# Kernel tuning notes

Hardware: AMD Instinct MI355X
Metric: run time of the kernel (lower is better)

The kernel has to match this reference:

```python
import jax, jax.numpy as jnp
import numpy as np
import math

ALPHA, BETA = 0.0, 0.1  # MarketRelation defaults


def setup_inputs() -> dict:
    key = jax.random.key(0)
    ks = jax.random.split(key, 15)
    n, T, d, K, C = 1024, 8, 64, 8, 64
    h = d  # hidden = (2*infeat)//2 = infeat
    s = 0.1
    u = jax.random.uniform(ks[13], (n, n, K), jnp.float32, 1e-6, 1.0 - 1e-6)
    return {
        "x":   jax.random.normal(ks[0], (n, T, d), jnp.float32),
        "Ind": jax.random.uniform(ks[1], (n, n), jnp.float32),
        "Loc": jax.random.uniform(ks[2], (n, n), jnp.float32),
        "a":   jax.random.normal(ks[3], (T, 1), jnp.float32),
        "W1m": jax.random.normal(ks[4], (2 * d, h), jnp.float32) * s,
        "b1m": jax.random.normal(ks[5], (h,), jnp.float32) * s,
        "W2m": jax.random.normal(ks[6], (h, 1), jnp.float32) * s,
        "b2m": jax.random.normal(ks[7], (1,), jnp.float32) * s,
        "W1s": jax.random.normal(ks[8], (2 * d, h), jnp.float32) * s,
        "b1s": jax.random.normal(ks[9], (h,), jnp.float32) * s,
        "W2s": jax.random.normal(ks[10], (h, K), jnp.float32) * s,
        "b2s": jax.random.normal(ks[11], (K,), jnp.float32) * s,
        "E":   jax.random.normal(ks[12], (K, n, C), jnp.float32) * s,
        "g":   -jnp.log(-jnp.log(u)),  # Gumbel(0,1) noise for gumbel_softmax
    }


def reference(x, Ind, Loc, a, W1m, b1m, W2m, b2m, W1s, b1s, W2s, b2s, E, g):
    n, T, d = x.shape
    # --- MarketRelation ---
    # fc1(concat(x_j, x_k)) == x_j @ W1m[:d] + x_k @ W1m[d:] + b1m (same math,
    # avoids materializing the N x N x 2d concat tensor)
    W1a, W1b = W1m[:d], W1m[d:]
    a_soft = jax.nn.softmax(a, axis=0)  # [T,1]
    A_mkt = jnp.zeros((n, n), x.dtype)
    for i in range(T):
        xi = x[:, i, :]                      # [n,d]
        hA = xi @ W1a                        # [n,h]
        hB = xi @ W1b                        # [n,h]
        hmat = jax.nn.relu(hA[:, None, :] + hB[None, :, :] + b1m)  # [n,n,h]
        adj = jax.nn.relu(hmat @ W2m + b2m)[..., 0]                # [n,n]
        factor = 1.0 + ALPHA * math.exp(-BETA * (T - i - 1))
        A_mkt = A_mkt + adj * (a_soft[i, 0] * factor)
    # --- NobsRelation (on last timestep) ---
    xl = x[:, -1, :]
    Ws1a, Ws1b = W1s[:d], W1s[d:]
    hs = jax.nn.relu((xl @ Ws1a)[:, None, :] + (xl @ Ws1b)[None, :, :] + b1s)
    logits = jax.nn.relu(hs @ W2s + b2s)          # [n,n,K]
    y = jax.nn.softmax(logits + g, axis=-1)       # gumbel_softmax, tau=1, soft
    D = jnp.einsum('knc,kmc->nmk', E, E)          # stack of E_k E_k^T, [n,n,K]
    A_nobs = jnp.sum(D * y, axis=-1)              # [n,n]
    return jnp.stack([Ind, Loc, A_mkt, A_nobs])   # [4,n,n]
```

## Files before the change

kernel.cpp:

```cpp
#include <hip/hip_runtime.h>

typedef unsigned short USH;
typedef float v2f __attribute__((ext_vector_type(2)));

__device__ __forceinline__ float bf2f(USH u) {
    return __uint_as_float(((unsigned int)u) << 16);
}
__device__ __forceinline__ USH f2bf(float f) {
    unsigned int i = __float_as_uint(f);
    i += 0x7FFFu + ((i >> 16) & 1u);
    return (USH)(i >> 16);
}
__device__ __forceinline__ v2f relu2(v2f s) {
    return __builtin_elementwise_max(s, (v2f)(0.0f));
}

__device__ __forceinline__ float ldf(const void* p, long idx, int bf) {
    return bf ? bf2f(((const USH*)p)[idx]) : ((const float*)p)[idx];
}
__device__ __forceinline__ void ld4(const void* p, long idx, int bf, float o[4]) {
    if (bf) {
        ushort4 u = *(const ushort4*)((const USH*)p + idx);
        o[0] = bf2f(u.x); o[1] = bf2f(u.y); o[2] = bf2f(u.z); o[3] = bf2f(u.w);
    } else {
        float4 v = *(const float4*)((const float*)p + idx);
        o[0] = v.x; o[1] = v.y; o[2] = v.z; o[3] = v.w;
    }
}

__device__ __forceinline__ int detect_bf(const void* ind) {
    const uint4* p = (const uint4*)ind;
    unsigned o = 0;
    #pragma unroll
    for (int i = 0; i < 8; ++i) { uint4 v = p[i]; o |= v.x | v.y | v.z | v.w; }
    return (o & 0x8000u) == 0;
}


__global__ __launch_bounds__(256) void k_pre_d(
    const void* __restrict__ x,
    const void* __restrict__ W1m,
    const void* __restrict__ b1m,
    const void* __restrict__ W1s,
    const void* __restrict__ b1s,
    const void* __restrict__ E,
    const void* __restrict__ IndDet,
    float* __restrict__ hAf,
    float* __restrict__ hBf,
    USH* __restrict__ D)
{
    __shared__ float smem[8192];
    float* sA = smem;
    float* sB = smem + 4096;
    const int bf = detect_bf(IndDet);
    const int tid = threadIdx.x;
    const int bid = blockIdx.x;
    const int tx = tid & 15, ty = tid >> 4;

    if (bid < 2048) {
        const int mb = (bid & 15) * 64, nb = ((bid >> 4) & 15) * 64, k = bid >> 8;
        const long ek = (long)k * 65536;
        {
            const int r_l = tid >> 2, cq = tid & 3;
            const long bn = ek + (long)(nb + r_l) * 64 + cq * 16;
            const long bm = ek + (long)(mb + r_l) * 64 + cq * 16;
            #pragma unroll
            for (int j = 0; j < 4; ++j) {
                const int c0 = cq * 16 + j * 4;
                float o[4];
                ld4(E, bn + j * 4, bf, o);
                #pragma unroll
                for (int e = 0; e < 4; ++e) sA[(c0 + e) * 64 + r_l] = o[e];
                ld4(E, bm + j * 4, bf, o);
                #pragma unroll
                for (int e = 0; e < 4; ++e) sB[(c0 + e) * 64 + r_l] = o[e];
            }
        }
        __syncthreads();
        const int m0 = tx * 4, n0 = ty * 4;
        v2f acc2[4][2] = {};
        #pragma unroll 8
        for (int c = 0; c < 64; ++c) {
            const float4 an = *(const float4*)&sA[c * 64 + n0];
            const float4 am = *(const float4*)&sB[c * 64 + m0];
            const float aa[4] = {an.x, an.y, an.z, an.w};
            v2f m01; m01.x = am.x; m01.y = am.y;
            v2f m23; m23.x = am.z; m23.y = am.w;
            #pragma unroll
            for (int ni = 0; ni < 4; ++ni) {
                const v2f av = (v2f)(aa[ni]);
                acc2[ni][0] = __builtin_elementwise_fma(av, m01, acc2[ni][0]);
                acc2[ni][1] = __builtin_elementwise_fma(av, m23, acc2[ni][1]);
            }
        }
        #pragma unroll
        for (int ni = 0; ni < 4; ++ni) {
            ushort4 o;
            o.x = f2bf(acc2[ni][0].x); o.y = f2bf(acc2[ni][0].y);
            o.z = f2bf(acc2[ni][1].x); o.w = f2bf(acc2[ni][1].y);
            *(ushort4*)&D[(long)k * 1048576 + (long)(nb + n0 + ni) * 1024 + mb + m0] = o;
        }
    } else {
        const int bid2 = bid - 2048;
        const int nbase = (bid2 & 15) * 64;
        const int by = bid2 >> 4;
        int t, rb;
        const void* Wsrc;
        const void* bias;
        float* dst;
        if (by < 8)        { t = by;     rb = 0;  Wsrc = W1m; bias = nullptr; dst = hAf + by * 65536; }
        else if (by < 16)  { t = by - 8; rb = 64; Wsrc = W1m; bias = b1m;     dst = hBf + (by - 8) * 65536; }
        else if (by == 16) { t = 7;      rb = 0;  Wsrc = W1s; bias = nullptr; dst = hAf + 8 * 65536; }
        else               { t = 7;      rb = 64; Wsrc = W1s; bias = b1s;     dst = hBf + 8 * 65536; }

        {
            const int n_l = tid >> 2, dq = tid & 3;
            const long base = (long)(nbase + n_l) * 512 + t * 64 + dq * 16;
            #pragma unroll
            for (int j = 0; j < 4; ++j) {
                float o[4]; ld4(x, base + j * 4, bf, o);
                const int d0 = dq * 16 + j * 4;
                #pragma unroll
                for (int e = 0; e < 4; ++e) sA[(d0 + e) * 64 + n_l] = o[e];
            }
        }
        {
            const int d_l = tid >> 2, cq = tid & 3;
            const long base = (long)(rb + d_l) * 64 + cq * 16;
            #pragma unroll
            for (int j = 0; j < 4; ++j) {
                float o[4]; ld4(Wsrc, base + j * 4, bf, o);
                const int c0 = cq * 16 + j * 4;
                #pragma unroll
                for (int e = 0; e < 4; ++e) sB[d_l * 64 + c0 + e] = o[e];
            }
        }
        __syncthreads();

        const int c0 = tx * 4, nq = ty * 4;
        float acc[4][4] = {};
        #pragma unroll 16
        for (int d = 0; d < 64; ++d) {
            const float4 xa = *(const float4*)&sA[d * 64 + nq];
            const float4 wv = *(const float4*)&sB[d * 64 + c0];
            const float aa[4] = {xa.x, xa.y, xa.z, xa.w};
            const float ww[4] = {wv.x, wv.y, wv.z, wv.w};
            #pragma unroll
            for (int ci = 0; ci < 4; ++ci)
                #pragma unroll
                for (int ni = 0; ni < 4; ++ni)
                    acc[ci][ni] += ww[ci] * aa[ni];
        }
        float b[4] = {0.f, 0.f, 0.f, 0.f};
        if (bias) {
            #pragma unroll
            for (int ci = 0; ci < 4; ++ci) b[ci] = ldf(bias, c0 + ci, bf);
        }
        #pragma unroll
        for (int ci = 0; ci < 4; ++ci) {
            float4 o;
            o.x = acc[ci][0] + b[ci]; o.y = acc[ci][1] + b[ci];
            o.z = acc[ci][2] + b[ci]; o.w = acc[ci][3] + b[ci];
            *(float4*)&dst[(c0 + ci) * 1024 + nbase + nq] = o;
        }
    }
}

__global__ __launch_bounds__(256, 2) void k_main(
    const float* __restrict__ hAf,
    const float* __restrict__ hBf,
    const USH* __restrict__ Dm,
    const void* __restrict__ Ind, const void* __restrict__ Loc,
    const void* __restrict__ a, const void* __restrict__ W2m,
    const void* __restrict__ b2m, const void* __restrict__ W2s,
    const void* __restrict__ b2s, const void* __restrict__ g,
    void* __restrict__ out)
{
    __shared__ float As[2][4096];
    __shared__ float Bs[2][2048];
    __shared__ float w2s_l[512];
    __shared__ float w2m_l[64];
    __shared__ float asoft_l[8];

    const int bf = detect_bf(Ind);
    const int tid = threadIdx.x;
    const int mb = blockIdx.x * 32, nb = blockIdx.y * 64;
    const int tx = tid & 15, ty = tid >> 4;
    const int n0 = ty * 4;
    const int m0 = tx * 2;

    const int cA = tid >> 4, qA = (tid & 15) * 4;
    const int cB = tid >> 3, qB = (tid & 7) * 4;

    if (tid < 64) w2m_l[tid] = ldf(W2m, tid, bf);
    if (tid >= 64 && tid < 192) {
        const int q = tid - 64;
        float o[4]; ld4(W2s, q * 4, bf, o);
        #pragma unroll
        for (int e = 0; e < 4; ++e) w2s_l[q * 4 + e] = o[e];
    }
    if (tid < 8) {
        float av[8], mx = -1e30f, s = 0.0f;
        #pragma unroll
        for (int k = 0; k < 8; ++k) { av[k] = ldf(a, k, bf); mx = fmaxf(mx, av[k]); }
        #pragma unroll
        for (int k = 0; k < 8; ++k) s += __expf(av[k] - mx);
        asoft_l[tid] = __expf(av[tid] - mx) / s;
    }
    const float b2m_f = ldf(b2m, 0, bf);

    #pragma unroll
    for (int p = 0; p < 4; ++p) {
        const int c = cA + p * 16;
        *(float4*)&As[0][c * 64 + qA] = *(const float4*)(hAf + (long)c * 1024 + nb + qA);
    }
    #pragma unroll
    for (int p = 0; p < 2; ++p) {
        const int c = cB + p * 32;
        *(float4*)&Bs[0][c * 32 + qB] = *(const float4*)(hBf + (long)c * 1024 + mb + qB);
    }
    __syncthreads();

    v2f amk[4] = {(v2f)(0.0f), (v2f)(0.0f), (v2f)(0.0f), (v2f)(0.0f)};

    for (int t = 0; t < 8; ++t) {
        const int cur = t & 1, nxt = cur ^ 1;
        const float* srcA = hAf + (long)(t + 1) * 65536;
        const float* srcB = hBf + (long)(t + 1) * 65536;
        float4 pfa[4], pfb[2];
        #pragma unroll
        for (int p = 0; p < 4; ++p)
            pfa[p] = *(const float4*)(srcA + (long)(cA + p * 16) * 1024 + nb + qA);
        #pragma unroll
        for (int p = 0; p < 2; ++p)
            pfb[p] = *(const float4*)(srcB + (long)(cB + p * 32) * 1024 + mb + qB);

        v2f acc[4] = {(v2f)(0.0f), (v2f)(0.0f), (v2f)(0.0f), (v2f)(0.0f)};
        const float* Ac = As[cur];
        const float* Bc = Bs[cur];
        #pragma unroll 4
        for (int c4 = 0; c4 < 16; ++c4) {
            const float4 wq = *(const float4*)&w2m_l[c4 * 4];
            const float ww[4] = {wq.x, wq.y, wq.z, wq.w};
            #pragma unroll
            for (int j = 0; j < 4; ++j) {
                const int c = c4 * 4 + j;
                const float4 aq = *(const float4*)&Ac[c * 64 + n0];
                const v2f bb = *(const v2f*)&Bc[c * 32 + m0];
                const float aa[4] = {aq.x, aq.y, aq.z, aq.w};
                const v2f wv = (v2f)(ww[j]);
                #pragma unroll
                for (int ni = 0; ni < 4; ++ni) {
                    const v2f s = relu2(bb + (v2f)(aa[ni]));
                    acc[ni] = __builtin_elementwise_fma(s, wv, acc[ni]);
                }
            }
        }
        const v2f asv = (v2f)(asoft_l[t]);
        const v2f b2v = (v2f)(b2m_f);
        #pragma unroll
        for (int ni = 0; ni < 4; ++ni)
            amk[ni] = __builtin_elementwise_fma(relu2(acc[ni] + b2v), asv, amk[ni]);

        #pragma unroll
        for (int p = 0; p < 4; ++p)
            *(float4*)&As[nxt][(cA + p * 16) * 64 + qA] = pfa[p];
        #pragma unroll
        for (int p = 0; p < 2; ++p)
            *(float4*)&Bs[nxt][(cB + p * 32) * 32 + qB] = pfb[p];
        __syncthreads();
    }

    v2f lgm[4][8];
    #pragma unroll
    for (int ni = 0; ni < 4; ++ni)
        #pragma unroll
        for (int k = 0; k < 8; ++k) lgm[ni][k] = (v2f)(0.0f);

    #pragma unroll 2
    for (int c4 = 0; c4 < 16; ++c4) {
        #pragma unroll
        for (int j = 0; j < 4; ++j) {
            const int c = c4 * 4 + j;
            const float4 aq = *(const float4*)&As[0][c * 64 + n0];
            const v2f bb = *(const v2f*)&Bs[0][c * 32 + m0];
            const float aa[4] = {aq.x, aq.y, aq.z, aq.w};
            const float4 wa = *(const float4*)&w2s_l[c * 8];
            const float4 wb = *(const float4*)&w2s_l[c * 8 + 4];
            const float wk[8] = {wa.x, wa.y, wa.z, wa.w, wb.x, wb.y, wb.z, wb.w};
            #pragma unroll
            for (int ni = 0; ni < 4; ++ni) {
                const v2f z = relu2(bb + (v2f)(aa[ni]));
                #pragma unroll
                for (int k = 0; k < 8; ++k)
                    lgm[ni][k] = __builtin_elementwise_fma(z, (v2f)(wk[k]), lgm[ni][k]);
            }
        }
    }

    float b2sv[8];
    #pragma unroll
    for (int k = 0; k < 8; ++k) b2sv[k] = ldf(b2s, k, bf);

    const int mg = mb + m0;
    #pragma unroll
    for (int ni = 0; ni < 4; ++ni) {
        const int n = nb + n0 + ni;
        const long rowoff = ((long)n << 10) + mg;
        float gv[16];
        ld4(g, rowoff * 8 + 0, bf, gv + 0);
        ld4(g, rowoff * 8 + 4, bf, gv + 4);
        ld4(g, rowoff * 8 + 8, bf, gv + 8);
        ld4(g, rowoff * 8 + 12, bf, gv + 12);

        float s0 = 0.0f, s1 = 0.0f, d0 = 0.0f, d1 = 0.0f;
        #pragma unroll
        for (int k = 0; k < 8; ++k) {
            const v2f lr = relu2(lgm[ni][k] + (v2f)(b2sv[k]));
            const float e0 = __expf(lr.x + gv[k]);
            const float e1 = __expf(lr.y + gv[8 + k]);
            s0 += e0; s1 += e1;
            const ushort2 dv = *(const ushort2*)&Dm[((long)k << 20) + rowoff];
            d0 += bf2f(dv.x) * e0;
            d1 += bf2f(dv.y) * e1;
        }

        if (bf) {
            USH* o = (USH*)out;
            *(ushort2*)&o[rowoff] = *(const ushort2*)&((const USH*)Ind)[rowoff];
            *(ushort2*)&o[1048576 + rowoff] = *(const ushort2*)&((const USH*)Loc)[rowoff];
            ushort2 o2; o2.x = f2bf(amk[ni].x); o2.y = f2bf(amk[ni].y);
            *(ushort2*)&o[2 * 1048576 + rowoff] = o2;
            ushort2 o3; o3.x = f2bf(d0 / s0); o3.y = f2bf(d1 / s1);
            *(ushort2*)&o[3 * 1048576 + rowoff] = o3;
        } else {
            float* o = (float*)out;
            *(float2*)&o[rowoff] = *(const float2*)&((const float*)Ind)[rowoff];
            *(float2*)&o[1048576 + rowoff] = *(const float2*)&((const float*)Loc)[rowoff];
            float2 o2; o2.x = amk[ni].x; o2.y = amk[ni].y;
            *(float2*)&o[2 * 1048576 + rowoff] = o2;
            float2 o3; o3.x = d0 / s0; o3.y = d1 / s1;
            *(float2*)&o[3 * 1048576 + rowoff] = o3;
        }
    }
}

extern "C" void kernel_launch(void* const* d_in, const int* in_sizes, int n_in,
                              void* d_out, int out_size, void* d_ws, size_t ws_size,
                              hipStream_t stream) {
    const void* x   = d_in[0];
    const void* Ind = d_in[1];
    const void* Loc = d_in[2];
    const void* a   = d_in[3];
    const void* W1m = d_in[4];
    const void* b1m = d_in[5];
    const void* W2m = d_in[6];
    const void* b2m = d_in[7];
    const void* W1s = d_in[8];
    const void* b1s = d_in[9];
    const void* W2s = d_in[10];
    const void* b2s = d_in[11];
    const void* E   = d_in[12];
    const void* g   = d_in[13];

    float* ws  = (float*)d_ws;
    float* hAf = ws;
    float* hBf = hAf + 589824;
    USH*   Dm  = (USH*)(hBf + 589824);

    k_pre_d<<<dim3(2336), 256, 0, stream>>>(x, W1m, b1m, W1s, b1s, E, Ind,
                                            hAf, hBf, Dm);
    k_main<<<dim3(32, 16), 256, 0, stream>>>(hAf, hBf, Dm,
                                             Ind, Loc, a, W2m, b2m, W2s, b2s,
                                             g, d_out);
}
```

Before: 193.9 us.

## Use packed fp16 dot2 for pairwise MLP and bf16 MFMA for E E^T

```diff
diff --git a/kernel.cpp b/kernel.cpp
--- a/kernel.cpp
+++ b/kernel.cpp
@@ -1,7 +1,11 @@
 #include <hip/hip_runtime.h>
 
 typedef unsigned short USH;
-typedef float v2f __attribute__((ext_vector_type(2)));
+typedef unsigned int UIN;
+typedef _Float16 F16;
+typedef F16 h2 __attribute__((ext_vector_type(2)));
+typedef short bfrag __attribute__((ext_vector_type(8)));
+typedef float f32x4 __attribute__((ext_vector_type(4)));
 
 __device__ __forceinline__ float bf2f(USH u) {
     return __uint_as_float(((unsigned int)u) << 16);
@@ -11,8 +15,23 @@
     i += 0x7FFFu + ((i >> 16) & 1u);
     return (USH)(i >> 16);
 }
-__device__ __forceinline__ v2f relu2(v2f s) {
-    return __builtin_elementwise_max(s, (v2f)(0.0f));
+__device__ __forceinline__ UIN pkh2(float a, float b) {
+    h2 h; h.x = (F16)a; h.y = (F16)b;
+    union { h2 hh; UIN u; } c; c.hh = h; return c.u;
+}
+__device__ __forceinline__ h2 U2H(UIN u) {
+    union { UIN u; h2 h; } c; c.u = u; return c.h;
+}
+__device__ __forceinline__ h2 relu2h(h2 s) {
+    const h2 zz = (h2)(F16)0.0f;
+    return __builtin_elementwise_max(s, zz);
+}
+__device__ __forceinline__ float fdot2(h2 a, h2 b, float c) {
+#if __has_builtin(__builtin_amdgcn_fdot2)
+    return __builtin_amdgcn_fdot2(a, b, c, false);
+#else
+    return c + (float)a.x * (float)b.x + (float)a.y * (float)b.y;
+#endif
 }
 
 __device__ __forceinline__ float ldf(const void* p, long idx, int bf) {
@@ -45,73 +64,105 @@
     const void* __restrict__ b1s,
     const void* __restrict__ E,
     const void* __restrict__ IndDet,
-    float* __restrict__ hAf,
-    float* __restrict__ hBf,
+    UIN* __restrict__ hA16,
+    UIN* __restrict__ hB16,
     USH* __restrict__ D)
 {
     __shared__ float smem[8192];
-    float* sA = smem;
-    float* sB = smem + 4096;
     const int bf = detect_bf(IndDet);
     const int tid = threadIdx.x;
     const int bid = blockIdx.x;
-    const int tx = tid & 15, ty = tid >> 4;
-
-    if (bid < 2048) {
-        const int mb = (bid & 15) * 64, nb = ((bid >> 4) & 15) * 64, k = bid >> 8;
+
+    if (bid < 512) {
+        USH* sE = (USH*)smem;
+        const int k = bid >> 6;
+        const int nb = ((bid >> 3) & 7) * 128, mb = (bid & 7) * 128;
         const long ek = (long)k * 65536;
-        {
-            const int r_l = tid >> 2, cq = tid & 3;
-            const long bn = ek + (long)(nb + r_l) * 64 + cq * 16;
-            const long bm = ek + (long)(mb + r_l) * 64 + cq * 16;
-            #pragma unroll
-            for (int j = 0; j < 4; ++j) {
-                const int c0 = cq * 16 + j * 4;
-                float o[4];
-                ld4(E, bn + j * 4, bf, o);
-                #pragma unroll
-                for (int e = 0; e < 4; ++e) sA[(c0 + e) * 64 + r_l] = o[e];
-                ld4(E, bm + j * 4, bf, o);
-                #pragma unroll
-                for (int e = 0; e < 4; ++e) sB[(c0 + e) * 64 + r_l] = o[e];
+
+        const int row = tid >> 1;
+        const int c0 = (tid & 1) * 32;
+        #pragma unroll
+        for (int side = 0; side < 2; ++side) {
+            const int rbase = side ? mb : nb;
+            USH* sDst = sE + side * 8192;
+            const long gbase = ek + (long)(rbase + row) * 64 + c0;
+            USH tmp[32];
+            if (bf) {
+                #pragma unroll
+                for (int q = 0; q < 4; ++q)
+                    *(uint4*)&tmp[q * 8] = *(const uint4*)((const USH*)E + gbase + q * 8);
+            } else {
+                #pragma unroll
+                for (int q = 0; q < 4; ++q) {
+                    const float4 va = *(const float4*)((const float*)E + gbase + q * 8);
+                    const float4 vb = *(const float4*)((const float*)E + gbase + q * 8 + 4);
+                    tmp[q * 8 + 0] = f2bf(va.x); tmp[q * 8 + 1] = f2bf(va.y);
+                    tmp[q * 8 + 2] = f2bf(va.z); tmp[q * 8 + 3] = f2bf(va.w);
+                    tmp[q * 8 + 4] = f2bf(vb.x); tmp[q * 8 + 5] = f2bf(vb.y);
+                    tmp[q * 8 + 6] = f2bf(vb.z); tmp[q * 8 + 7] = f2bf(vb.w);
+                }
+            }
+            #pragma unroll
+            for (int q = 0; q < 4; ++q) {
+                const int byte = (c0 + q * 8) * 2;
+                const int sw = (row * 128 + (byte ^ ((row & 7) << 4))) >> 1;
+                *(uint4*)&sDst[sw] = *(uint4*)&tmp[q * 8];
             }
         }
         __syncthreads();
-        const int m0 = tx * 4, n0 = ty * 4;
-        v2f acc2[4][2] = {};
-        #pragma unroll 8
-        for (int c = 0; c < 64; ++c) {
-            const float4 an = *(const float4*)&sA[c * 64 + n0];
-            const float4 am = *(const float4*)&sB[c * 64 + m0];
-            const float aa[4] = {an.x, an.y, an.z, an.w};
-            v2f m01; m01.x = am.x; m01.y = am.y;
-            v2f m23; m23.x = am.z; m23.y = am.w;
-            #pragma unroll
-            for (int ni = 0; ni < 4; ++ni) {
-                const v2f av = (v2f)(aa[ni]);
-                acc2[ni][0] = __builtin_elementwise_fma(av, m01, acc2[ni][0]);
-                acc2[ni][1] = __builtin_elementwise_fma(av, m23, acc2[ni][1]);
-            }
-        }
-        #pragma unroll
-        for (int ni = 0; ni < 4; ++ni) {
-            ushort4 o;
-            o.x = f2bf(acc2[ni][0].x); o.y = f2bf(acc2[ni][0].y);
-            o.z = f2bf(acc2[ni][1].x); o.w = f2bf(acc2[ni][1].y);
-            *(ushort4*)&D[(long)k * 1048576 + (long)(nb + n0 + ni) * 1024 + mb + m0] = o;
+
+        const int lane = tid & 63;
+        const int w = tid >> 6;
+        const int wn = (w >> 1) * 64, wm = (w & 1) * 64;
+        const int fr = lane & 15, kg = lane >> 4;
+
+        f32x4 acc[4][4] = {};
+        #pragma unroll
+        for (int ks = 0; ks < 2; ++ks) {
+            const int cb = (ks * 32 + kg * 8) * 2;
+            bfrag af[4], bfv[4];
+            #pragma unroll
+            for (int f = 0; f < 4; ++f) {
+                const int ra = wn + f * 16 + fr;
+                af[f] = *(const bfrag*)&sE[(ra * 128 + (cb ^ ((ra & 7) << 4))) >> 1];
+                const int rb = wm + f * 16 + fr;
+                bfv[f] = *(const bfrag*)&sE[8192 + ((rb * 128 + (cb ^ ((rb & 7) << 4))) >> 1)];
+            }
+            #pragma unroll
+            for (int fn = 0; fn < 4; ++fn)
+                #pragma unroll
+                for (int fm = 0; fm < 4; ++fm)
+                    acc[fn][fm] = __builtin_amdgcn_mfma_f32_16x16x32_bf16(
+                        af[fn], bfv[fm], acc[fn][fm], 0, 0, 0);
+        }
+
+        USH* Dk = D + ((long)k << 20);
+        #pragma unroll
+        for (int fn = 0; fn < 4; ++fn) {
+            const int nrow = nb + wn + fn * 16 + kg * 4;
+            #pragma unroll
+            for (int fm = 0; fm < 4; ++fm) {
+                const int mcol = mb + wm + fm * 16 + fr;
+                #pragma unroll
+                for (int r = 0; r < 4; ++r)
+                    Dk[(long)(nrow + r) * 1024 + mcol] = f2bf(acc[fn][fm][r]);
+            }
         }
     } else {
-        const int bid2 = bid - 2048;
+        float* sA = smem;
+        float* sB = smem + 4096;
+        const int tx = tid & 15, ty = tid >> 4;
+        const int bid2 = bid - 512;
         const int nbase = (bid2 & 15) * 64;
         const int by = bid2 >> 4;
         int t, rb;
         const void* Wsrc;
         const void* bias;
-        float* dst;
-        if (by < 8)        { t = by;     rb = 0;  Wsrc = W1m; bias = nullptr; dst = hAf + by * 65536; }
-        else if (by < 16)  { t = by - 8; rb = 64; Wsrc = W1m; bias = b1m;     dst = hBf + (by - 8) * 65536; }
-        else if (by == 16) { t = 7;      rb = 0;  Wsrc = W1s; bias = nullptr; dst = hAf + 8 * 65536; }
-        else               { t = 7;      rb = 64; Wsrc = W1s; bias = b1s;     dst = hBf + 8 * 65536; }
+        UIN* dst;
+        if (by < 8)        { t = by;     rb = 0;  Wsrc = W1m; bias = nullptr; dst = hA16 + by * 32768; }
+        else if (by < 16)  { t = by - 8; rb = 64; Wsrc = W1m; bias = b1m;     dst = hB16 + (by - 8) * 32768; }
+        else if (by == 16) { t = 7;      rb = 0;  Wsrc = W1s; bias = nullptr; dst = hA16 + 8 * 32768; }
+        else               { t = 7;      rb = 64; Wsrc = W1s; bias = b1s;     dst = hB16 + 8 * 32768; }
 
         {
             const int n_l = tid >> 2, dq = tid & 3;
@@ -156,19 +207,19 @@
             #pragma unroll
             for (int ci = 0; ci < 4; ++ci) b[ci] = ldf(bias, c0 + ci, bf);
         }
-        #pragma unroll
-        for (int ci = 0; ci < 4; ++ci) {
-            float4 o;
-            o.x = acc[ci][0] + b[ci]; o.y = acc[ci][1] + b[ci];
-            o.z = acc[ci][2] + b[ci]; o.w = acc[ci][3] + b[ci];
-            *(float4*)&dst[(c0 + ci) * 1024 + nbase + nq] = o;
-        }
-    }
-}
-
-__global__ __launch_bounds__(256, 2) void k_main(
-    const float* __restrict__ hAf,
-    const float* __restrict__ hBf,
+        const int cp0 = c0 >> 1;
+        #pragma unroll
+        for (int ni = 0; ni < 4; ++ni) {
+            const int col = nbase + nq + ni;
+            dst[cp0 * 1024 + col]       = pkh2(acc[0][ni] + b[0], acc[1][ni] + b[1]);
+            dst[(cp0 + 1) * 1024 + col] = pkh2(acc[2][ni] + b[2], acc[3][ni] + b[3]);
+        }
+    }
+}
+
+__global__ __launch_bounds__(256, 4) void k_main(
+    const UIN* __restrict__ hA16,
+    const UIN* __restrict__ hB16,
     const USH* __restrict__ Dm,
     const void* __restrict__ Ind, const void* __restrict__ Loc,
     const void* __restrict__ a, const void* __restrict__ W2m,
@@ -176,28 +227,30 @@
     const void* __restrict__ b2s, const void* __restrict__ g,
     void* __restrict__ out)
 {
-    __shared__ float As[2][4096];
-    __shared__ float Bs[2][2048];
-    __shared__ float w2s_l[512];
-    __shared__ float w2m_l[64];
+    __shared__ UIN As[2][1024];
+    __shared__ UIN Bs[2][1024];
+    __shared__ UIN w2m16[32];
+    __shared__ UIN w2s16[256];
     __shared__ float asoft_l[8];
 
     const int bf = detect_bf(Ind);
     const int tid = threadIdx.x;
-    const int mb = blockIdx.x * 32, nb = blockIdx.y * 64;
+    const int mb = blockIdx.x * 32, nb = blockIdx.y * 32;
     const int tx = tid & 15, ty = tid >> 4;
-    const int n0 = ty * 4;
-    const int m0 = tx * 2;
-
-    const int cA = tid >> 4, qA = (tid & 15) * 4;
-    const int cB = tid >> 3, qB = (tid & 7) * 4;
-
-    if (tid < 64) w2m_l[tid] = ldf(W2m, tid, bf);
-    if (tid >= 64 && tid < 192) {
+    const int n0 = ty * 2, m0 = tx * 2;
+
+    const int cpS = tid >> 3, q4 = (tid & 7) * 4;
+
+    if (tid < 32) w2m16[tid] = pkh2(ldf(W2m, 2 * tid, bf), ldf(W2m, 2 * tid + 1, bf));
+    if (tid >= 64 && tid < 128) {
         const int q = tid - 64;
-        float o[4]; ld4(W2s, q * 4, bf, o);
-        #pragma unroll
-        for (int e = 0; e < 4; ++e) w2s_l[q * 4 + e] = o[e];
+        const int cp = q >> 1, kh = (q & 1) * 4;
+        #pragma unroll
+        for (int e = 0; e < 4; ++e) {
+            const int k = kh + e;
+            w2s16[cp * 8 + k] = pkh2(ldf(W2s, (2 * cp) * 8 + k, bf),
+                                     ldf(W2s, (2 * cp + 1) * 8 + k, bf));
+        }
     }
     if (tid < 8) {
         float av[8], mx = -1e30f, s = 0.0f;
@@ -209,92 +262,67 @@
     }
     const float b2m_f = ldf(b2m, 0, bf);
 
-    #pragma unroll
-    for (int p = 0; p < 4; ++p) {
-        const int c = cA + p * 16;
-        *(float4*)&As[0][c * 64 + qA] = *(const float4*)(hAf + (long)c * 1024 + nb + qA);
-    }
-    #pragma unroll
-    for (int p = 0; p < 2; ++p) {
-        const int c = cB + p * 32;
-        *(float4*)&Bs[0][c * 32 + qB] = *(const float4*)(hBf + (long)c * 1024 + mb + qB);
-    }
+    *(uint4*)&As[0][cpS * 32 + q4] = *(const uint4*)(hA16 + cpS * 1024 + nb + q4);
+    *(uint4*)&Bs[0][cpS * 32 + q4] = *(const uint4*)(hB16 + cpS * 1024 + mb + q4);
     __syncthreads();
 
-    v2f amk[4] = {(v2f)(0.0f), (v2f)(0.0f), (v2f)(0.0f), (v2f)(0.0f)};
+    float amk[2][2] = {{0.f, 0.f}, {0.f, 0.f}};
 
     for (int t = 0; t < 8; ++t) {
         const int cur = t & 1, nxt = cur ^ 1;
-        const float* srcA = hAf + (long)(t + 1) * 65536;
-        const float* srcB = hBf + (long)(t + 1) * 65536;
-        float4 pfa[4], pfb[2];
-        #pragma unroll
-        for (int p = 0; p < 4; ++p)
-            pfa[p] = *(const float4*)(srcA + (long)(cA + p * 16) * 1024 + nb + qA);
-        #pragma unroll
-        for (int p = 0; p < 2; ++p)
-            pfb[p] = *(const float4*)(srcB + (long)(cB + p * 32) * 1024 + mb + qB);
-
-        v2f acc[4] = {(v2f)(0.0f), (v2f)(0.0f), (v2f)(0.0f), (v2f)(0.0f)};
-        const float* Ac = As[cur];
-        const float* Bc = Bs[cur];
-        #pragma unroll 4
-        for (int c4 = 0; c4 < 16; ++c4) {
-            const float4 wq = *(const float4*)&w2m_l[c4 * 4];
-            const float ww[4] = {wq.x, wq.y, wq.z, wq.w};
-            #pragma unroll
-            for (int j = 0; j < 4; ++j) {
-                const int c = c4 * 4 + j;
-                const float4 aq = *(const float4*)&Ac[c * 64 + n0];
-                const v2f bb = *(const v2f*)&Bc[c * 32 + m0];
-                const float aa[4] = {aq.x, aq.y, aq.z, aq.w};
-                const v2f wv = (v2f)(ww[j]);
-                #pragma unroll
-                for (int ni = 0; ni < 4; ++ni) {
-                    const v2f s = relu2(bb + (v2f)(aa[ni]));
-                    acc[ni] = __builtin_elementwise_fma(s, wv, acc[ni]);
-                }
-            }
-        }
-        const v2f asv = (v2f)(asoft_l[t]);
-        const v2f b2v = (v2f)(b2m_f);
-        #pragma unroll
-        for (int ni = 0; ni < 4; ++ni)
-            amk[ni] = __builtin_elementwise_fma(relu2(acc[ni] + b2v), asv, amk[ni]);
-
-        #pragma unroll
-        for (int p = 0; p < 4; ++p)
-            *(float4*)&As[nxt][(cA + p * 16) * 64 + qA] = pfa[p];
-        #pragma unroll
-        for (int p = 0; p < 2; ++p)
-            *(float4*)&Bs[nxt][(cB + p * 32) * 32 + qB] = pfb[p];
+        const uint4 pa = *(const uint4*)(hA16 + (t + 1) * 32768 + cpS * 1024 + nb + q4);
+        const uint4 pb = *(const uint4*)(hB16 + (t + 1) * 32768 + cpS * 1024 + mb + q4);
+
+        float a00 = 0.f, a01 = 0.f, a10 = 0.f, a11 = 0.f;
+        #pragma unroll
+        for (int cp = 0; cp < 32; ++cp) {
+            const uint2 au = *(const uint2*)&As[cur][cp * 32 + n0];
+            const uint2 bu = *(const uint2*)&Bs[cur][cp * 32 + m0];
+            const h2 wv = U2H(w2m16[cp]);
+            const h2 ha0 = U2H(au.x), ha1 = U2H(au.y);
+            const h2 hb0 = U2H(bu.x), hb1 = U2H(bu.y);
+            const h2 z00 = relu2h(ha0 + hb0), z01 = relu2h(ha0 + hb1);
+            const h2 z10 = relu2h(ha1 + hb0), z11 = relu2h(ha1 + hb1);
+            a00 = fdot2(z00, wv, a00); a01 = fdot2(z01, wv, a01);
+            a10 = fdot2(z10, wv, a10); a11 = fdot2(z11, wv, a11);
+        }
+        const float as_t = asoft_l[t];
+        amk[0][0] += fmaxf(a00 + b2m_f, 0.f) * as_t;
+        amk[0][1] += fmaxf(a01 + b2m_f, 0.f) * as_t;
+        amk[1][0] += fmaxf(a10 + b2m_f, 0.f) * as_t;
+        amk[1][1] += fmaxf(a11 + b2m_f, 0.f) * as_t;
+
+        *(uint4*)&As[nxt][cpS * 32 + q4] = pa;
+        *(uint4*)&Bs[nxt][cpS * 32 + q4] = pb;
         __syncthreads();
     }
 
-    v2f lgm[4][8];
+    float lg[2][2][8];
     #pragma unroll
-    for (int ni = 0; ni < 4; ++ni)
-        #pragma unroll
-        for (int k = 0; k < 8; ++k) lgm[ni][k] = (v2f)(0.0f);
-
-    #pragma unroll 2
-    for (int c4 = 0; c4 < 16; ++c4) {
-        #pragma unroll
-        for (int j = 0; j < 4; ++j) {
-            const int c = c4 * 4 + j;
-            const float4 aq = *(const float4*)&As[0][c * 64 + n0];
-            const v2f bb = *(const v2f*)&Bs[0][c * 32 + m0];
-            const float aa[4] = {aq.x, aq.y, aq.z, aq.w};
-            const float4 wa = *(const float4*)&w2s_l[c * 8];
-            const float4 wb = *(const float4*)&w2s_l[c * 8 + 4];
-            const float wk[8] = {wa.x, wa.y, wa.z, wa.w, wb.x, wb.y, wb.z, wb.w};
-            #pragma unroll
-            for (int ni = 0; ni < 4; ++ni) {
-                const v2f z = relu2(bb + (v2f)(aa[ni]));
-                #pragma unroll
-                for (int k = 0; k < 8; ++k)
-                    lgm[ni][k] = __builtin_elementwise_fma(z, (v2f)(wk[k]), lgm[ni][k]);
-            }
+    for (int i = 0; i < 2; ++i)
+        #pragma unroll
+        for (int j = 0; j < 2; ++j)
+            #pragma unroll
+            for (int k = 0; k < 8; ++k) lg[i][j][k] = 0.f;
+
+    #pragma unroll
+    for (int cp = 0; cp < 32; ++cp) {
+        const uint2 au = *(const uint2*)&As[0][cp * 32 + n0];
+        const uint2 bu = *(const uint2*)&Bs[0][cp * 32 + m0];
+        const h2 ha0 = U2H(au.x), ha1 = U2H(au.y);
+        const h2 hb0 = U2H(bu.x), hb1 = U2H(bu.y);
+        const h2 z00 = relu2h(ha0 + hb0), z01 = relu2h(ha0 + hb1);
+        const h2 z10 = relu2h(ha1 + hb0), z11 = relu2h(ha1 + hb1);
+        const uint4 wa = *(const uint4*)&w2s16[cp * 8];
+        const uint4 wb = *(const uint4*)&w2s16[cp * 8 + 4];
+        const UIN wk[8] = {wa.x, wa.y, wa.z, wa.w, wb.x, wb.y, wb.z, wb.w};
+        #pragma unroll
+        for (int k = 0; k < 8; ++k) {
+            const h2 wv = U2H(wk[k]);
+            lg[0][0][k] = fdot2(z00, wv, lg[0][0][k]);
+            lg[0][1][k] = fdot2(z01, wv, lg[0][1][k]);
+            lg[1][0][k] = fdot2(z10, wv, lg[1][0][k]);
+            lg[1][1][k] = fdot2(z11, wv, lg[1][1][k]);
         }
     }
 
@@ -304,7 +332,7 @@
 
     const int mg = mb + m0;
     #pragma unroll
-    for (int ni = 0; ni < 4; ++ni) {
+    for (int ni = 0; ni < 2; ++ni) {
         const int n = nb + n0 + ni;
         const long rowoff = ((long)n << 10) + mg;
         float gv[16];
@@ -316,9 +344,10 @@
         float s0 = 0.0f, s1 = 0.0f, d0 = 0.0f, d1 = 0.0f;
         #pragma unroll
         for (int k = 0; k < 8; ++k) {
-            const v2f lr = relu2(lgm[ni][k] + (v2f)(b2sv[k]));
-            const float e0 = __expf(lr.x + gv[k]);
-            const float e1 = __expf(lr.y + gv[8 + k]);
+            const float l0 = fmaxf(lg[ni][0][k] + b2sv[k], 0.f);
+            const float l1 = fmaxf(lg[ni][1][k] + b2sv[k], 0.f);
+            const float e0 = __expf(l0 + gv[k]);
+            const float e1 = __expf(l1 + gv[8 + k]);
             s0 += e0; s1 += e1;
             const ushort2 dv = *(const ushort2*)&Dm[((long)k << 20) + rowoff];
             d0 += bf2f(dv.x) * e0;
@@ -329,7 +358,7 @@
             USH* o = (USH*)out;
             *(ushort2*)&o[rowoff] = *(const ushort2*)&((const USH*)Ind)[rowoff];
             *(ushort2*)&o[1048576 + rowoff] = *(const ushort2*)&((const USH*)Loc)[rowoff];
-            ushort2 o2; o2.x = f2bf(amk[ni].x); o2.y = f2bf(amk[ni].y);
+            ushort2 o2; o2.x = f2bf(amk[ni][0]); o2.y = f2bf(amk[ni][1]);
             *(ushort2*)&o[2 * 1048576 + rowoff] = o2;
             ushort2 o3; o3.x = f2bf(d0 / s0); o3.y = f2bf(d1 / s1);
             *(ushort2*)&o[3 * 1048576 + rowoff] = o3;
@@ -337,7 +366,7 @@
             float* o = (float*)out;
             *(float2*)&o[rowoff] = *(const float2*)&((const float*)Ind)[rowoff];
             *(float2*)&o[1048576 + rowoff] = *(const float2*)&((const float*)Loc)[rowoff];
-            float2 o2; o2.x = amk[ni].x; o2.y = amk[ni].y;
+            float2 o2; o2.x = amk[ni][0]; o2.y = amk[ni][1];
             *(float2*)&o[2 * 1048576 + rowoff] = o2;
             float2 o3; o3.x = d0 / s0; o3.y = d1 / s1;
             *(float2*)&o[3 * 1048576 + rowoff] = o3;
@@ -363,14 +392,14 @@
     const void* E   = d_in[12];
     const void* g   = d_in[13];
 
-    float* ws  = (float*)d_ws;
-    float* hAf = ws;
-    float* hBf = hAf + 589824;
-    USH*   Dm  = (USH*)(hBf + 589824);
-
-    k_pre_d<<<dim3(2336), 256, 0, stream>>>(x, W1m, b1m, W1s, b1s, E, Ind,
-                                            hAf, hBf, Dm);
-    k_main<<<dim3(32, 16), 256, 0, stream>>>(hAf, hBf, Dm,
+    UIN* ws   = (UIN*)d_ws;
+    UIN* hA16 = ws;
+    UIN* hB16 = hA16 + 294912;
+    USH* Dm   = (USH*)(hB16 + 294912);
+
+    k_pre_d<<<dim3(800), 256, 0, stream>>>(x, W1m, b1m, W1s, b1s, E, Ind,
+                                           hA16, hB16, Dm);
+    k_main<<<dim3(32, 32), 256, 0, stream>>>(hA16, hB16, Dm,
                                              Ind, Loc, a, W2m, b2m, W2s, b2s,
                                              g, d_out);
 }
```

New measurement: 398.1 us. +105.3%, slower.
